# Performance work log

Measured on AMD Instinct MI355X. Metric: run time of the kernel, lower is better.

## Reference

```python
import jax, jax.numpy as jnp
import numpy as np

# Path weights from e3nn FullyConnectedTensorProduct with irrep_normalization='component',
# path_normalization='element': alpha = dim(1e)=3 divided by sum of path fan-ins (5*1 + 1*1 = 6)
# => path_weight = sqrt(0.5) for both instructions.
# wigner_3j(0,1,1) = I/sqrt(3); wigner_3j(1,1,1) = eps_{ijk}/sqrt(6) (Levi-Civita).
C01 = float(np.sqrt(0.5) / np.sqrt(3.0))
C11 = float(np.sqrt(0.5) / np.sqrt(6.0))


def setup_inputs() -> dict:
    key = jax.random.key(0)
    ks = jax.random.split(key, 8)
    B, N = 1024, 4096
    feats = jax.random.normal(ks[0], (B, N, 8), dtype=jnp.float32)      # 5x0e + 1x1e
    edge_attr = jax.random.normal(ks[1], (B, N, 3), dtype=jnp.float32)  # 1x1e
    # TP weights: path (5x0e x 1x1e -> 1x1e) has shape (5,1,1) -> (5,);
    # path (1x1e x 1x1e -> 1x1e) has shape (1,1,1) -> (1,).
    w_path0 = jax.random.normal(ks[2], (5,), dtype=jnp.float32)
    w_path1 = jax.random.normal(ks[3], (1,), dtype=jnp.float32)
    # MLP params (nn.Linear style: y = x @ W + b)
    W1 = jax.random.normal(ks[4], (3, 128), dtype=jnp.float32) / np.sqrt(3.0)
    b1 = jnp.zeros((128,), dtype=jnp.float32)
    W2 = jax.random.normal(ks[5], (128, 3), dtype=jnp.float32) / np.sqrt(128.0)
    b2 = jnp.zeros((3,), dtype=jnp.float32)
    return {"feats": feats, "edge_attr": edge_attr,
            "w_path0": w_path0, "w_path1": w_path1,
            "W1": W1, "b1": b1, "W2": W2, "b2": b2}


def reference(feats, edge_attr, w_path0, w_path1, W1, b1, W2, b2):
    # FullyConnectedTensorProduct(5x0e+1x1e, 1x1e -> 1x1e)
    x1_scalars = feats[..., :5]   # [B,N,5]  5x0e
    x1_vec = feats[..., 5:8]      # [B,N,3]  1x1e
    # path 0: scalars gate the edge vector
    s = jnp.einsum('bnu,u->bn', x1_scalars, w_path0)            # [B,N]
    # path 1: cross product of the two l=1 vectors
    tp_out = (C01 * s[..., None] * edge_attr
              + (C11 * w_path1[0]) * jnp.cross(x1_vec, edge_attr))  # [B,N,3]
    # mean pool over nodes -> graph embedding [B,3]
    g = tp_out.mean(axis=1)
    h = jax.nn.relu(g @ W1 + b1)   # [B,128]
    return h @ W2 + b2             # [B,3]
```

## Files before the change

### kernel.cpp

```cpp
#include <hip/hip_runtime.h>

constexpr int B = 1024;
constexpr int N = 4096;
constexpr int CHUNKS = 16;
constexpr int BLK = 256;
constexpr float C01 = 0.4082482904638630f;
constexpr float C11 = 0.2886751345948129f;

__global__ __launch_bounds__(BLK) void tp_reduce_kernel(
    const float* __restrict__ feats,
    const float* __restrict__ edge_attr,
    const float* __restrict__ w_path0,
    const float* __restrict__ w_path1,
    float* __restrict__ part)
{
    const int blk   = blockIdx.x;
    const int b     = blk >> 4;
    const int chunk = blk & (CHUNKS - 1);
    const int n     = chunk * BLK + threadIdx.x;
    const long idx  = (long)b * N + n;

    const float4* fp = reinterpret_cast<const float4*>(feats + idx * 8);
    float4 f0 = fp[0];
    float4 f1 = fp[1];

    const float* ep = edge_attr + idx * 3;
    float e0 = ep[0], e1 = ep[1], e2 = ep[2];

    float s = f0.x * w_path0[0] + f0.y * w_path0[1] + f0.z * w_path0[2]
            + f0.w * w_path0[3] + f1.x * w_path0[4];
    float v0 = f1.y, v1 = f1.z, v2 = f1.w;
    float c11w = C11 * w_path1[0];
    float c01s = C01 * s;

    float t0 = c01s * e0 + c11w * (v1 * e2 - v2 * e1);
    float t1 = c01s * e1 + c11w * (v2 * e0 - v0 * e2);
    float t2 = c01s * e2 + c11w * (v0 * e1 - v1 * e0);

    __shared__ float r0[BLK], r1[BLK], r2[BLK];
    int t = threadIdx.x;
    r0[t] = t0; r1[t] = t1; r2[t] = t2;
    __syncthreads();
    #pragma unroll
    for (int off = BLK / 2; off > 0; off >>= 1) {
        if (t < off) {
            r0[t] += r0[t + off];
            r1[t] += r1[t + off];
            r2[t] += r2[t + off];
        }
        __syncthreads();
    }
    if (t == 0) {
        float* p = part + (long)blk * 3;
        p[0] = r0[0];
        p[1] = r1[0];
        p[2] = r2[0];
    }
}

__global__ __launch_bounds__(128) void mlp_kernel(
    const float* __restrict__ part,
    const float* __restrict__ W1,
    const float* __restrict__ b1,
    const float* __restrict__ W2,
    const float* __restrict__ b2,
    float* __restrict__ out)
{
    const int b = blockIdx.x;
    const int j = threadIdx.x;

    __shared__ float g[3];
    if (j < 3) {
        float acc = 0.0f;
        const float* p = part + (long)b * CHUNKS * 3 + j;
        #pragma unroll
        for (int c = 0; c < CHUNKS; ++c) acc += p[c * 3];
        g[j] = acc * (1.0f / (float)N);
    }
    __syncthreads();

    float h = b1[j] + g[0] * W1[j] + g[1] * W1[128 + j] + g[2] * W1[256 + j];
    h = fmaxf(h, 0.0f);

    __shared__ float red[3][128];
    red[0][j] = h * W2[j * 3 + 0];
    red[1][j] = h * W2[j * 3 + 1];
    red[2][j] = h * W2[j * 3 + 2];
    __syncthreads();
    #pragma unroll
    for (int off = 64; off > 0; off >>= 1) {
        if (j < off) {
            red[0][j] += red[0][j + off];
            red[1][j] += red[1][j + off];
            red[2][j] += red[2][j + off];
        }
        __syncthreads();
    }
    if (j < 3) out[(long)b * 3 + j] = red[j][0] + b2[j];
}

extern "C" void kernel_launch(void* const* d_in, const int* in_sizes, int n_in,
                              void* d_out, int out_size, void* d_ws, size_t ws_size,
                              hipStream_t stream) {
    const float* feats     = (const float*)d_in[0];
    const float* edge_attr = (const float*)d_in[1];
    const float* w_path0   = (const float*)d_in[2];
    const float* w_path1   = (const float*)d_in[3];
    const float* W1        = (const float*)d_in[4];
    const float* b1        = (const float*)d_in[5];
    const float* W2        = (const float*)d_in[6];
    const float* b2        = (const float*)d_in[7];
    float* out = (float*)d_out;

    float* part = (float*)d_ws;

    tp_reduce_kernel<<<B * CHUNKS, BLK, 0, stream>>>(feats, edge_attr, w_path0,
                                                     w_path1, part);
    mlp_kernel<<<B, 128, 0, stream>>>(part, W1, b1, W2, b2, out);
}
```

Baseline: 35.38 us.

## Fuse tensor-product reduction and MLP into one kernel with per-graph blocks

Replaces the two-kernel pipeline (chunked reduction writing partials, then an MLP kernel) with a single kernel in which one block handles a whole graph. Each thread loops over groups of 4 nodes, using wide float4 loads for both feats and edge_attr, and accumulates in registers. Reductions use wave shuffles in place of shared-memory tree loops. This removes a kernel launch, the partial-sum round trip through global memory and many barriers. The grid drops to 1024 blocks, so there is less parallelism per graph, and each thread carries more per-iteration work.

```diff
diff --git a/kernel.cpp b/kernel.cpp
--- a/kernel.cpp
+++ b/kernel.cpp
@@ -1,102 +1,111 @@
 #include <hip/hip_runtime.h>
 
-constexpr int B = 1024;
-constexpr int N = 4096;
-constexpr int CHUNKS = 16;
+constexpr int B   = 1024;
+constexpr int N   = 4096;
 constexpr int BLK = 256;
+constexpr int VPT = 4;
+constexpr int GROUPS = N / (BLK * VPT);
 constexpr float C01 = 0.4082482904638630f;
 constexpr float C11 = 0.2886751345948129f;
 
-__global__ __launch_bounds__(BLK) void tp_reduce_kernel(
+__global__ __launch_bounds__(BLK) void fused_kernel(
     const float* __restrict__ feats,
     const float* __restrict__ edge_attr,
     const float* __restrict__ w_path0,
     const float* __restrict__ w_path1,
-    float* __restrict__ part)
-{
-    const int blk   = blockIdx.x;
-    const int b     = blk >> 4;
-    const int chunk = blk & (CHUNKS - 1);
-    const int n     = chunk * BLK + threadIdx.x;
-    const long idx  = (long)b * N + n;
-
-    const float4* fp = reinterpret_cast<const float4*>(feats + idx * 8);
-    float4 f0 = fp[0];
-    float4 f1 = fp[1];
-
-    const float* ep = edge_attr + idx * 3;
-    float e0 = ep[0], e1 = ep[1], e2 = ep[2];
-
-    float s = f0.x * w_path0[0] + f0.y * w_path0[1] + f0.z * w_path0[2]
-            + f0.w * w_path0[3] + f1.x * w_path0[4];
-    float v0 = f1.y, v1 = f1.z, v2 = f1.w;
-    float c11w = C11 * w_path1[0];
-    float c01s = C01 * s;
-
-    float t0 = c01s * e0 + c11w * (v1 * e2 - v2 * e1);
-    float t1 = c01s * e1 + c11w * (v2 * e0 - v0 * e2);
-    float t2 = c01s * e2 + c11w * (v0 * e1 - v1 * e0);
-
-    __shared__ float r0[BLK], r1[BLK], r2[BLK];
-    int t = threadIdx.x;
-    r0[t] = t0; r1[t] = t1; r2[t] = t2;
-    __syncthreads();
-    #pragma unroll
-    for (int off = BLK / 2; off > 0; off >>= 1) {
-        if (t < off) {
-            r0[t] += r0[t + off];
-            r1[t] += r1[t + off];
-            r2[t] += r2[t + off];
-        }
-        __syncthreads();
-    }
-    if (t == 0) {
-        float* p = part + (long)blk * 3;
-        p[0] = r0[0];
-        p[1] = r1[0];
-        p[2] = r2[0];
-    }
-}
-
-__global__ __launch_bounds__(128) void mlp_kernel(
-    const float* __restrict__ part,
     const float* __restrict__ W1,
     const float* __restrict__ b1,
     const float* __restrict__ W2,
     const float* __restrict__ b2,
     float* __restrict__ out)
 {
-    const int b = blockIdx.x;
-    const int j = threadIdx.x;
+    const int b   = blockIdx.x;
+    const int tid = threadIdx.x;
 
-    __shared__ float g[3];
-    if (j < 3) {
-        float acc = 0.0f;
-        const float* p = part + (long)b * CHUNKS * 3 + j;
+    const float w0 = w_path0[0], w1 = w_path0[1], w2 = w_path0[2],
+                w3 = w_path0[3], w4 = w_path0[4];
+    const float c11w = C11 * w_path1[0];
+
+    float acc0 = 0.0f, acc1 = 0.0f, acc2 = 0.0f;
+
+    for (int grp = 0; grp < GROUPS; ++grp) {
+        const int n0 = grp * (BLK * VPT) + tid * VPT;
+        const long idx = (long)b * N + n0;
+
+        const float4* fp = reinterpret_cast<const float4*>(feats + idx * 8);
+        float4 F[8];
         #pragma unroll
-        for (int c = 0; c < CHUNKS; ++c) acc += p[c * 3];
-        g[j] = acc * (1.0f / (float)N);
+        for (int i = 0; i < 8; ++i) F[i] = fp[i];
+        const float* f = reinterpret_cast<const float*>(F);
+
+        const float4* ep = reinterpret_cast<const float4*>(edge_attr + idx * 3);
+        float4 E[3];
+        #pragma unroll
+        for (int i = 0; i < 3; ++i) E[i] = ep[i];
+        const float* e = reinterpret_cast<const float*>(E);
+
+        #pragma unroll
+        for (int k = 0; k < VPT; ++k) {
+            const float* fk = f + k * 8;
+            const float* ek = e + k * 3;
+            float s = fk[0] * w0 + fk[1] * w1 + fk[2] * w2 + fk[3] * w3 + fk[4] * w4;
+            float c01s = C01 * s;
+            float v0 = fk[5], v1 = fk[6], v2 = fk[7];
+            float e0 = ek[0], e1 = ek[1], e2 = ek[2];
+            acc0 += c01s * e0 + c11w * (v1 * e2 - v2 * e1);
+            acc1 += c01s * e1 + c11w * (v2 * e0 - v0 * e2);
+            acc2 += c01s * e2 + c11w * (v0 * e1 - v1 * e0);
+        }
+    }
+
+    #pragma unroll
+    for (int off = 32; off > 0; off >>= 1) {
+        acc0 += __shfl_down(acc0, off);
+        acc1 += __shfl_down(acc1, off);
+        acc2 += __shfl_down(acc2, off);
+    }
+
+    __shared__ float wsum[4][3];
+    const int wave = tid >> 6;
+    const int lane = tid & 63;
+    if (lane == 0) {
+        wsum[wave][0] = acc0;
+        wsum[wave][1] = acc1;
+        wsum[wave][2] = acc2;
     }
     __syncthreads();
 
-    float h = b1[j] + g[0] * W1[j] + g[1] * W1[128 + j] + g[2] * W1[256 + j];
-    h = fmaxf(h, 0.0f);
+    __shared__ float g[3];
+    if (tid < 3) {
+        g[tid] = (wsum[0][tid] + wsum[1][tid] + wsum[2][tid] + wsum[3][tid])
+               * (1.0f / (float)N);
+    }
+    __syncthreads();
 
-    __shared__ float red[3][128];
-    red[0][j] = h * W2[j * 3 + 0];
-    red[1][j] = h * W2[j * 3 + 1];
-    red[2][j] = h * W2[j * 3 + 2];
+    float p0 = 0.0f, p1 = 0.0f, p2 = 0.0f;
+    if (tid < 128) {
+        float h = b1[tid] + g[0] * W1[tid] + g[1] * W1[128 + tid] + g[2] * W1[256 + tid];
+        h = fmaxf(h, 0.0f);
+        p0 = h * W2[tid * 3 + 0];
+        p1 = h * W2[tid * 3 + 1];
+        p2 = h * W2[tid * 3 + 2];
+    }
+    #pragma unroll
+    for (int off = 32; off > 0; off >>= 1) {
+        p0 += __shfl_down(p0, off);
+        p1 += __shfl_down(p1, off);
+        p2 += __shfl_down(p2, off);
+    }
+    __shared__ float pr[4][3];
+    if (lane == 0) {
+        pr[wave][0] = p0;
+        pr[wave][1] = p1;
+        pr[wave][2] = p2;
+    }
     __syncthreads();
-    #pragma unroll
-    for (int off = 64; off > 0; off >>= 1) {
-        if (j < off) {
-            red[0][j] += red[0][j + off];
-            red[1][j] += red[1][j + off];
-            red[2][j] += red[2][j + off];
-        }
-        __syncthreads();
+    if (tid < 3) {
+        out[(long)b * 3 + tid] = pr[0][tid] + pr[1][tid] + b2[tid];
     }
-    if (j < 3) out[(long)b * 3 + j] = red[j][0] + b2[j];
 }
 
 extern "C" void kernel_launch(void* const* d_in, const int* in_sizes, int n_in,
@@ -112,9 +121,6 @@
     const float* b2        = (const float*)d_in[7];
     float* out = (float*)d_out;
 
-    float* part = (float*)d_ws;
-
-    tp_reduce_kernel<<<B * CHUNKS, BLK, 0, stream>>>(feats, edge_attr, w_path0,
-                                                     w_path1, part);
-    mlp_kernel<<<B, 128, 0, stream>>>(part, W1, b1, W2, b2, out);
+    fused_kernel<<<B, BLK, 0, stream>>>(feats, edge_attr, w_path0, w_path1,
+                                        W1, b1, W2, b2, out);
 }
```

Measured after the change: 87.35 us. 147% more time.
